# Performance work log

Measured on AMD Instinct MI355X. Metric: run time of the kernel, lower is better.

Reference implementation:

```python
import jax, jax.numpy as jnp
import numpy as np

BETA = 0.1
NUM_LAYERS = 2  # GT layers inside each FastGTN


def densify(edge_index, edge_weight, num_nodes):
    # edge_index: [T, 2, E] int, edge_weight: [T, E] -> dense [T, N, N]
    T, _, E = edge_index.shape
    t_ids = jnp.broadcast_to(jnp.arange(T)[:, None], (T, E))
    dense = jnp.zeros((T, num_nodes, num_nodes), dtype=edge_weight.dtype)
    return dense.at[t_ids, edge_index[:, 0, :], edge_index[:, 1, :]].add(edge_weight)


def fast_gtn(dense_A, X, Ws, conv_w, lin_w, lin_b, num_nodes):
    # Ws: [C, w_in, w_out]; conv_w: [L, C, T]; lin_w: [C*w_out, w_out]
    H = jnp.einsum('nk,ckh->cnh', X, Ws)              # [C, N, w_out]
    X_ = jax.lax.stop_gradient(H)                      # clone().detach()
    for l in range(NUM_LAYERS):
        filt = jax.nn.softmax(conv_w[l], axis=1)       # [C, T]
        adj = jnp.einsum('ct,tij->cij', filt, dense_A) # [C, N, N]
        H = jnp.einsum('cij,cjh->cih', adj, H)         # graph conv per channel
    H_ = jax.nn.relu(BETA * X_ + (1.0 - BETA) * H)     # [C, N, w_out]
    H_ = jnp.transpose(H_, (1, 0, 2)).reshape(num_nodes, -1)  # [N, C*w_out]
    return jax.nn.relu(H_ @ lin_w + lin_b)             # [N, w_out]


def setup_inputs() -> dict:
    key = jax.random.key(0)
    ks = jax.random.split(key, 12)
    T, E, N = 4, 131072, 4096
    C, F_IN, H_OUT = 2, 128, 64
    edge_index = jax.random.randint(ks[0], (T, 2, E), 0, N, dtype=jnp.int64)
    edge_weight = jax.random.uniform(ks[1], (T, E), dtype=jnp.float32)
    X = jax.random.normal(ks[2], (N, F_IN), dtype=jnp.float32)
    def glorot(k, shape):
        fan_in, fan_out = shape[-2], shape[-1]
        s = jnp.sqrt(6.0 / (fan_in + fan_out))
        return jax.random.uniform(k, shape, jnp.float32, -s, s)
    # FastGTN #1 (w_in=F_IN)
    Ws1 = glorot(ks[3], (C, F_IN, H_OUT))
    conv_w1 = 0.1 * jax.random.normal(ks[4], (NUM_LAYERS, C, T), dtype=jnp.float32)
    lin_w1 = glorot(ks[5], (C * H_OUT, H_OUT))
    lin_b1 = jnp.zeros((H_OUT,), jnp.float32)
    # FastGTN #2 (w_in=H_OUT)
    Ws2 = glorot(ks[6], (C, H_OUT, H_OUT))
    conv_w2 = 0.1 * jax.random.normal(ks[7], (NUM_LAYERS, C, T), dtype=jnp.float32)
    lin_w2 = glorot(ks[8], (C * H_OUT, H_OUT))
    lin_b2 = jnp.zeros((H_OUT,), jnp.float32)
    return {"edge_index": edge_index, "edge_weight": edge_weight, "X": X,
            "Ws1": Ws1, "conv_w1": conv_w1, "lin_w1": lin_w1, "lin_b1": lin_b1,
            "Ws2": Ws2, "conv_w2": conv_w2, "lin_w2": lin_w2, "lin_b2": lin_b2}


def reference(edge_index, edge_weight, X, Ws1, conv_w1, lin_w1, lin_b1,
              Ws2, conv_w2, lin_w2, lin_b2):
    N = X.shape[0]
    dense_A = densify(edge_index, edge_weight, N)      # [T, N, N]
    H = fast_gtn(dense_A, X, Ws1, conv_w1, lin_w1, lin_b1, N)
    H = fast_gtn(dense_A, H, Ws2, conv_w2, lin_w2, lin_b2, N)
    return H
```

## Files before the change

kernel.cpp:

```cpp
#include <hip/hip_runtime.h>

#define E_EDGES 131072
#define N_NODES 4096
#define HOUT    64
#define NE_TOT  (4 * E_EDGES)
#define CAP     256
#define CSTRIDE 16

__device__ __forceinline__ unsigned short f2bf(float x) {
    unsigned u = __float_as_uint(x);
    return (unsigned short)((u + 0x7FFFu + ((u >> 16) & 1u)) >> 16);
}
__device__ __forceinline__ float bf2f(unsigned b) {
    return __uint_as_float(b << 16);
}

__device__ __forceinline__ void softmax4(const float* __restrict__ cw,
                                         int layer, int c, float f[4]) {
#pragma unroll
    for (int t = 0; t < 4; ++t) f[t] = cw[(layer * 2 + c) * 4 + t];
    float m = fmaxf(fmaxf(f[0], f[1]), fmaxf(f[2], f[3]));
    float s = 0.f;
#pragma unroll
    for (int t = 0; t < 4; ++t) { f[t] = expf(f[t] - m); s += f[t]; }
    float inv = 1.0f / s;
#pragma unroll
    for (int t = 0; t < 4; ++t) f[t] *= inv;
}

__device__ __forceinline__ float selw(const float f[4], int t) {
    float a = (t & 1) ? f[1] : f[0];
    float b = (t & 1) ? f[3] : f[2];
    return (t & 2) ? b : a;
}

__device__ __forceinline__ void fma8(float acc[8], float w, uint4 v) {
    acc[0] += w * bf2f(v.x & 0xFFFFu); acc[1] += w * bf2f(v.x >> 16);
    acc[2] += w * bf2f(v.y & 0xFFFFu); acc[3] += w * bf2f(v.y >> 16);
    acc[4] += w * bf2f(v.z & 0xFFFFu); acc[5] += w * bf2f(v.z >> 16);
    acc[6] += w * bf2f(v.w & 0xFFFFu); acc[7] += w * bf2f(v.w >> 16);
}

__device__ __forceinline__ uint4 pack8(const float acc[8]) {
    uint4 r;
    r.x = (unsigned)f2bf(acc[0]) | ((unsigned)f2bf(acc[1]) << 16);
    r.y = (unsigned)f2bf(acc[2]) | ((unsigned)f2bf(acc[3]) << 16);
    r.z = (unsigned)f2bf(acc[4]) | ((unsigned)f2bf(acc[5]) << 16);
    r.w = (unsigned)f2bf(acc[6]) | ((unsigned)f2bf(acc[7]) << 16);
    return r;
}

__device__ __forceinline__ void spmm_row2c(const unsigned* __restrict__ rowe, int len,
                                           const unsigned* __restrict__ Hc0,
                                           const unsigned* __restrict__ Hc1,
                                           const float f0[4], const float f1[4],
                                           int lane, float a0[8], float a1[8]) {
    int g  = lane >> 3;
    int hq = lane & 7;
#pragma unroll
    for (int j = 0; j < 8; ++j) { a0[j] = 0.f; a1[j] = 0.f; }
    int e = 0;
    for (; e + 16 <= len; e += 16) {
        unsigned r0 = rowe[e + g];
        unsigned r1 = rowe[e + 8 + g];
        int   d0 = r0 & 0xFFF, t0 = (r0 >> 12) & 3;
        int   d1 = r1 & 0xFFF, t1 = (r1 >> 12) & 3;
        float w0 = bf2f(r0 >> 16), w1 = bf2f(r1 >> 16);
        uint4 v00 = ((const uint4*)(Hc0 + d0 * (HOUT / 2)))[hq];
        uint4 v01 = ((const uint4*)(Hc1 + d0 * (HOUT / 2)))[hq];
        uint4 v10 = ((const uint4*)(Hc0 + d1 * (HOUT / 2)))[hq];
        uint4 v11 = ((const uint4*)(Hc1 + d1 * (HOUT / 2)))[hq];
        fma8(a0, w0 * selw(f0, t0), v00);
        fma8(a1, w0 * selw(f1, t0), v01);
        fma8(a0, w1 * selw(f0, t1), v10);
        fma8(a1, w1 * selw(f1, t1), v11);
    }
    for (; e + 8 <= len; e += 8) {
        unsigned r0 = rowe[e + g];
        int   d0 = r0 & 0xFFF, t0 = (r0 >> 12) & 3;
        float w0 = bf2f(r0 >> 16);
        uint4 v00 = ((const uint4*)(Hc0 + d0 * (HOUT / 2)))[hq];
        uint4 v01 = ((const uint4*)(Hc1 + d0 * (HOUT / 2)))[hq];
        fma8(a0, w0 * selw(f0, t0), v00);
        fma8(a1, w0 * selw(f1, t0), v01);
    }
    if (g < len - e) {
        unsigned r0 = rowe[e + g];
        int   d0 = r0 & 0xFFF, t0 = (r0 >> 12) & 3;
        float w0 = bf2f(r0 >> 16);
        uint4 v00 = ((const uint4*)(Hc0 + d0 * (HOUT / 2)))[hq];
        uint4 v01 = ((const uint4*)(Hc1 + d0 * (HOUT / 2)))[hq];
        fma8(a0, w0 * selw(f0, t0), v00);
        fma8(a1, w0 * selw(f1, t0), v01);
    }
#pragma unroll
    for (int j = 0; j < 8; ++j) {
        a0[j] += __shfl_xor(a0[j], 8);
        a0[j] += __shfl_xor(a0[j], 16);
        a0[j] += __shfl_xor(a0[j], 32);
        a1[j] += __shfl_xor(a1[j], 8);
        a1[j] += __shfl_xor(a1[j], 16);
        a1[j] += __shfl_xor(a1[j], 32);
    }
}

__global__ void __launch_bounds__(256)
zinit_kernel(const float* __restrict__ X, const float* __restrict__ Ws,
             float* __restrict__ H0, unsigned* __restrict__ H016,
             int* __restrict__ cursor) {
    int idx = blockIdx.x * 256 + threadIdx.x;
    if (idx < N_NODES * CSTRIDE) cursor[idx] = 0;
    int h = idx & 63;
    int n = (idx >> 6) & (N_NODES - 1);
    int c = idx >> 18;
    const float4* xv = (const float4*)(X + n * 128);
    const float*  w  = Ws + c * 128 * HOUT + h;
    float acc = 0.f;
#pragma unroll 8
    for (int k4 = 0; k4 < 32; ++k4) {
        float4 xx = xv[k4];
        acc += xx.x * w[(k4 * 4 + 0) * HOUT];
        acc += xx.y * w[(k4 * 4 + 1) * HOUT];
        acc += xx.z * w[(k4 * 4 + 2) * HOUT];
        acc += xx.w * w[(k4 * 4 + 3) * HOUT];
    }
    H0[idx] = acc;
    ((unsigned short*)H016)[idx] = f2bf(acc);
}

__global__ void __launch_bounds__(256)
scatter_kernel(const int* __restrict__ ei, const float* __restrict__ ew,
               int* __restrict__ cursor, unsigned* __restrict__ edges) {
    int i4 = (blockIdx.x * 256 + threadIdx.x) * 4;
    int t = i4 >> 17;
    int e = i4 & (E_EDGES - 1);
    int4   srcs = *(const int4*)(ei + (t * 2 + 0) * E_EDGES + e);
    int4   dsts = *(const int4*)(ei + (t * 2 + 1) * E_EDGES + e);
    float4 wts  = *(const float4*)(ew + t * E_EDGES + e);
    unsigned tb = (unsigned)t << 12;
    unsigned rec[4];
    int pos[4];
#pragma unroll
    for (int j = 0; j < 4; ++j)
        pos[j] = atomicAdd(&cursor[(&srcs.x)[j] * CSTRIDE], 1);
#pragma unroll
    for (int j = 0; j < 4; ++j) {
        rec[j] = ((unsigned)f2bf((&wts.x)[j]) << 16) | tb | (unsigned)(&dsts.x)[j];
        if (pos[j] < CAP)
            edges[(&srcs.x)[j] * CAP + pos[j]] = rec[j];
    }
}

__global__ void __launch_bounds__(256)
spmm_kernel(const int* __restrict__ cnt, const unsigned* __restrict__ edges,
            const unsigned* __restrict__ Hin16, unsigned* __restrict__ Hout16,
            const float* __restrict__ cw) {
    int row  = (blockIdx.x * 256 + threadIdx.x) >> 6;
    int lane = threadIdx.x & 63;
    float f0[4], f1[4];
    softmax4(cw, 0, 0, f0);
    softmax4(cw, 0, 1, f1);
    int len = min(cnt[row * CSTRIDE], CAP);
    float a0[8], a1[8];
    spmm_row2c(edges + row * CAP, len,
               Hin16, Hin16 + N_NODES * (HOUT / 2), f0, f1, lane, a0, a1);
    if ((lane >> 3) == 0) {
        int hq = lane & 7;
        ((uint4*)(Hout16 + row * (HOUT / 2)))[hq] = pack8(a0);
        ((uint4*)(Hout16 + (N_NODES + row) * (HOUT / 2)))[hq] = pack8(a1);
    }
}

template <bool FINAL>
__global__ void __launch_bounds__(256)
tail_kernel(const int* __restrict__ cnt, const unsigned* __restrict__ edges,
            const unsigned* __restrict__ Hin16,
            const float* __restrict__ H0,
            const float* __restrict__ cw,
            const float* __restrict__ lw, const float* __restrict__ lb,
            const float* __restrict__ Wsn,
            float* __restrict__ outp, unsigned* __restrict__ out16) {
    __shared__ float hcomb[4][2 * HOUT];
    __shared__ float mids[4][HOUT];
    int tid  = threadIdx.x;
    int r    = tid >> 6;
    int lane = tid & 63;
    int row  = blockIdx.x * 4 + r;

    float f0[4], f1[4];
    softmax4(cw, 1, 0, f0);
    softmax4(cw, 1, 1, f1);
    int len = min(cnt[row * CSTRIDE], CAP);
    float a0[8], a1[8];
    spmm_row2c(edges + row * CAP, len,
               Hin16, Hin16 + N_NODES * (HOUT / 2), f0, f1, lane, a0, a1);

    if ((lane >> 3) == 0) {
        int hq = lane & 7;
#pragma unroll
        for (int j = 0; j < 8; ++j) {
            int h = hq * 8 + j;
            float h00 = H0[row * HOUT + h];
            float h01 = H0[(N_NODES + row) * HOUT + h];
            hcomb[r][h]        = fmaxf(0.1f * h00 + 0.9f * a0[j], 0.f);
            hcomb[r][HOUT + h] = fmaxf(0.1f * h01 + 0.9f * a1[j], 0.f);
        }
    }
    __syncthreads();

    float a = lb[lane];
#pragma unroll 8
    for (int j = 0; j < 2 * HOUT; ++j) a += hcomb[r][j] * lw[j * HOUT + lane];

    if (FINAL) {
        outp[row * HOUT + lane] = fmaxf(a, 0.f);
    } else {
        mids[r][lane] = fmaxf(a, 0.f);
        __syncthreads();
#pragma unroll
        for (int c = 0; c < 2; ++c) {
            float acc = 0.f;
            const float* w = Wsn + c * HOUT * HOUT + lane;
#pragma unroll 8
            for (int k = 0; k < HOUT; ++k) acc += mids[r][k] * w[k * HOUT];
            int o = (c * N_NODES + row) * HOUT + lane;
            outp[o] = acc;
            ((unsigned short*)out16)[o] = f2bf(acc);
        }
    }
}

extern "C" void kernel_launch(void* const* d_in, const int* in_sizes, int n_in,
                              void* d_out, int out_size, void* d_ws, size_t ws_size,
                              hipStream_t stream) {
    const int*   ei  = (const int*)d_in[0];
    const float* ew  = (const float*)d_in[1];
    const float* X   = (const float*)d_in[2];
    const float* Ws1 = (const float*)d_in[3];
    const float* cw1 = (const float*)d_in[4];
    const float* lw1 = (const float*)d_in[5];
    const float* lb1 = (const float*)d_in[6];
    const float* Ws2 = (const float*)d_in[7];
    const float* cw2 = (const float*)d_in[8];
    const float* lw2 = (const float*)d_in[9];
    const float* lb2 = (const float*)d_in[10];
    float* outp = (float*)d_out;

    char* ws = (char*)d_ws;
    size_t off = 0;
    auto alloc = [&](size_t bytes) -> void* {
        void* p = ws + off;
        off += (bytes + 255) & ~size_t(255);
        return p;
    };
    int*      cursor = (int*)alloc((size_t)N_NODES * CSTRIDE * 4);
    unsigned* edges  = (unsigned*)alloc((size_t)N_NODES * CAP * 4);
    float*    H0a    = (float*)alloc((size_t)2 * N_NODES * HOUT * 4);
    unsigned* H0a16  = (unsigned*)alloc((size_t)2 * N_NODES * HOUT * 2);
    unsigned* Ha16   = (unsigned*)alloc((size_t)2 * N_NODES * HOUT * 2);
    float*    H0b    = (float*)alloc((size_t)2 * N_NODES * HOUT * 4);
    unsigned* H0b16  = (unsigned*)alloc((size_t)2 * N_NODES * HOUT * 2);

    zinit_kernel  <<<2048, 256, 0, stream>>>(X, Ws1, H0a, H0a16, cursor);
    scatter_kernel<<<NE_TOT / 1024, 256, 0, stream>>>(ei, ew, cursor, edges);

    spmm_kernel<<<1024, 256, 0, stream>>>(cursor, edges, H0a16, Ha16, cw1);
    tail_kernel<false><<<1024, 256, 0, stream>>>(
        cursor, edges, Ha16, H0a, cw1, lw1, lb1, Ws2, H0b, H0b16);

    spmm_kernel<<<1024, 256, 0, stream>>>(cursor, edges, H0b16, Ha16, cw2);
    tail_kernel<true><<<1024, 256, 0, stream>>>(
        cursor, edges, Ha16, H0b, cw2, lw2, lb2, nullptr, outp, nullptr);
}
```

Baseline: 112.2 us.

## Aggregate scatter atomics via per-block shared-memory histogram before global reservation

```diff
diff --git a/kernel.cpp b/kernel.cpp
--- a/kernel.cpp
+++ b/kernel.cpp
@@ -6,6 +6,10 @@
 #define NE_TOT  (4 * E_EDGES)
 #define CAP     256
 #define CSTRIDE 16
+#define SC_NBLK 64
+#define SC_NTHR 1024
+#define SC_EPB  (NE_TOT / SC_NBLK)
+#define SC_EPT  (SC_EPB / SC_NTHR)
 
 __device__ __forceinline__ unsigned short f2bf(float x) {
     unsigned u = __float_as_uint(x);
@@ -128,26 +132,46 @@
     ((unsigned short*)H016)[idx] = f2bf(acc);
 }
 
-__global__ void __launch_bounds__(256)
+__global__ void __launch_bounds__(SC_NTHR)
 scatter_kernel(const int* __restrict__ ei, const float* __restrict__ ew,
-               int* __restrict__ cursor, unsigned* __restrict__ edges) {
-    int i4 = (blockIdx.x * 256 + threadIdx.x) * 4;
-    int t = i4 >> 17;
-    int e = i4 & (E_EDGES - 1);
-    int4   srcs = *(const int4*)(ei + (t * 2 + 0) * E_EDGES + e);
-    int4   dsts = *(const int4*)(ei + (t * 2 + 1) * E_EDGES + e);
-    float4 wts  = *(const float4*)(ew + t * E_EDGES + e);
+               int* __restrict__ gcursor, unsigned* __restrict__ edges) {
+    __shared__ int shist[N_NODES];
+    __shared__ int sbase[N_NODES];
+    int tid = threadIdx.x;
+    int t   = blockIdx.x >> 4;
+    int e0  = (blockIdx.x & 15) * SC_EPB + tid * SC_EPT;
+    const int*   ps = ei + (t * 2 + 0) * E_EDGES + e0;
+    const int*   pd = ei + (t * 2 + 1) * E_EDGES + e0;
+    const float* pw = ew + t * E_EDGES + e0;
+#pragma unroll
+    for (int j = 0; j < 4; ++j) shist[tid * 4 + j] = 0;
+    __syncthreads();
+
+    int4   s0 = ((const int4*)ps)[0],  s1 = ((const int4*)ps)[1];
+    int4   d0 = ((const int4*)pd)[0],  d1 = ((const int4*)pd)[1];
+    float4 w0 = ((const float4*)pw)[0], w1 = ((const float4*)pw)[1];
+    int   srcs[8] = {s0.x, s0.y, s0.z, s0.w, s1.x, s1.y, s1.z, s1.w};
+    int   dsts[8] = {d0.x, d0.y, d0.z, d0.w, d1.x, d1.y, d1.z, d1.w};
+    float wts[8]  = {w0.x, w0.y, w0.z, w0.w, w1.x, w1.y, w1.z, w1.w};
+    int lpos[8];
+#pragma unroll
+    for (int j = 0; j < 8; ++j) lpos[j] = atomicAdd(&shist[srcs[j]], 1);
+    __syncthreads();
+
+#pragma unroll
+    for (int j = 0; j < 4; ++j) {
+        int b = tid * 4 + j;
+        int cntb = shist[b];
+        if (cntb) sbase[b] = atomicAdd(&gcursor[b * CSTRIDE], cntb);
+    }
+    __syncthreads();
+
     unsigned tb = (unsigned)t << 12;
-    unsigned rec[4];
-    int pos[4];
-#pragma unroll
-    for (int j = 0; j < 4; ++j)
-        pos[j] = atomicAdd(&cursor[(&srcs.x)[j] * CSTRIDE], 1);
-#pragma unroll
-    for (int j = 0; j < 4; ++j) {
-        rec[j] = ((unsigned)f2bf((&wts.x)[j]) << 16) | tb | (unsigned)(&dsts.x)[j];
-        if (pos[j] < CAP)
-            edges[(&srcs.x)[j] * CAP + pos[j]] = rec[j];
+#pragma unroll
+    for (int j = 0; j < 8; ++j) {
+        unsigned p = (unsigned)(sbase[srcs[j]] + lpos[j]);
+        unsigned rec = ((unsigned)f2bf(wts[j]) << 16) | tb | (unsigned)dsts[j];
+        if (p < CAP) edges[srcs[j] * CAP + p] = rec;
     }
 }
 
@@ -262,7 +286,7 @@
     unsigned* H0b16  = (unsigned*)alloc((size_t)2 * N_NODES * HOUT * 2);
 
     zinit_kernel  <<<2048, 256, 0, stream>>>(X, Ws1, H0a, H0a16, cursor);
-    scatter_kernel<<<NE_TOT / 1024, 256, 0, stream>>>(ei, ew, cursor, edges);
+    scatter_kernel<<<SC_NBLK, SC_NTHR, 0, stream>>>(ei, ew, cursor, edges);
 
     spmm_kernel<<<1024, 256, 0, stream>>>(cursor, edges, H0a16, Ha16, cw1);
     tail_kernel<false><<<1024, 256, 0, stream>>>(
```

After: 105.0 us. 6.4% less time.
